# Performance work log

Measured on AMD Instinct MI355X. Metric: run time of the kernel, lower is better.

The kernel has to match this reference:

```python
import jax, jax.numpy as jnp
import numpy as np

B, D_IN, D_H = 262144, 128, 128
PROJ_EPS = 1e-5  # ball projection epsilon (c = 1.0)


def _norm(x):
    return jnp.linalg.norm(x, axis=-1, keepdims=True)


def logmap0(x):
    # atanh(||x||) * x / ||x||, safe at 0 (c = 1)
    n = _norm(x)
    ns = jnp.where(n == 0, 0.5, n)
    return jnp.where(n == 0, jnp.zeros_like(x), jnp.arctanh(ns) * x / ns)


def expmap0(v):
    # tanh(||v||) * v / ||v||, safe at 0 (c = 1)
    n = _norm(v)
    ns = jnp.where(n == 0, 1.0, n)
    return jnp.where(n == 0, jnp.zeros_like(v), jnp.tanh(ns) * v / ns)


def proj(x):
    # clip back inside the unit Poincare ball
    n = _norm(x)
    maxnorm = 1.0 - PROJ_EPS
    ns = jnp.where(n == 0, 1.0, n)
    return jnp.where(n > maxnorm, x / ns * maxnorm, x)


def setup_inputs() -> dict:
    key = jax.random.key(0)
    ks = jax.random.split(key, 8)
    scale = 0.03  # keep points well inside the ball: ||x|| ~ 0.03*sqrt(128) ~ 0.34
    x = scale * jax.random.normal(ks[0], (B, D_IN), dtype=jnp.float32)
    h = scale * jax.random.normal(ks[1], (B, D_H), dtype=jnp.float32)
    fan_in = D_IN + D_H
    w_std = 1.0 / np.sqrt(fan_in)
    Wr = w_std * jax.random.normal(ks[2], (fan_in, D_H), dtype=jnp.float32)
    br = w_std * jax.random.normal(ks[3], (D_H,), dtype=jnp.float32)
    Wz = w_std * jax.random.normal(ks[4], (fan_in, D_H), dtype=jnp.float32)
    bz = w_std * jax.random.normal(ks[5], (D_H,), dtype=jnp.float32)
    Wh = w_std * jax.random.normal(ks[6], (fan_in, D_H), dtype=jnp.float32)
    bh = w_std * jax.random.normal(ks[7], (D_H,), dtype=jnp.float32)
    return {"x": x, "h": h, "Wr": Wr, "br": br, "Wz": Wz, "bz": bz, "Wh": Wh, "bh": bh}


def reference(x, h, Wr, br, Wz, bz, Wh, bh):
    x_tan = logmap0(x)            # [B, D_IN]
    h_tan = logmap0(h)            # [B, D_H]
    xh = jnp.concatenate([x_tan, h_tan], axis=1)  # [B, D_IN+D_H]
    r = jax.nn.sigmoid(xh @ Wr + br)
    z = jax.nn.sigmoid(xh @ Wz + bz)
    xh_reset = jnp.concatenate([x_tan, r * h_tan], axis=1)
    h_tilde = jnp.tanh(xh_reset @ Wh + bh)
    h_new_tan = (1.0 - z) * h_tan + z * h_tilde
    return proj(expmap0(h_new_tan))  # [B, D_H]
```

## Files before the change

kernel.cpp:

```cpp
#include <hip/hip_runtime.h>
#include <hip/hip_bf16.h>

typedef __attribute__((ext_vector_type(4))) float f32x4;
typedef __attribute__((ext_vector_type(8))) short bf16x8;
typedef __attribute__((ext_vector_type(4))) short bf16x4;
typedef __attribute__((ext_vector_type(2))) unsigned int u32x2;

#define D 128
#define BM 64

__device__ __forceinline__ unsigned short f2bf(float f){
  union { float f; unsigned int i; } c; c.f = f;
  unsigned int i = c.i;
  i += 0x7fffu + ((i >> 16) & 1u);
  return (unsigned short)(i >> 16);
}
__device__ __forceinline__ float bf2f(unsigned short u){
  union { float f; unsigned int i; } c; c.i = ((unsigned int)u) << 16; return c.f;
}
__device__ __forceinline__ unsigned int pk2(float a, float b){
  __hip_bfloat162 t = __float22bfloat162_rn(make_float2(a, b));
  return *reinterpret_cast<unsigned int*>(&t);
}
__device__ __forceinline__ float rcp_f(float x){ return __builtin_amdgcn_rcpf(x); }
__device__ __forceinline__ float exp2_f(float x){ return __builtin_amdgcn_exp2f(x); }
__device__ __forceinline__ float sigmoid_f(float t){
  return rcp_f(1.0f + exp2_f(-1.442695041f * t));
}
__device__ __forceinline__ float tanh_f(float t){
  return __builtin_fmaf(2.0f, rcp_f(1.0f + exp2_f(-2.885390082f * t)), -1.0f);
}

__global__ void prep_weights(const float* __restrict__ Wr, const float* __restrict__ Wz,
                             const float* __restrict__ Wh, unsigned short* __restrict__ wp)
{
  int w = blockIdx.x >> 6;
  int f = blockIdx.x & 63;
  int l = threadIdx.x;
  const float* src = (w == 0) ? Wr : ((w == 1) ? Wz : Wh);
  int nf = f >> 3, kk = f & 7;
  int col = nf * 16 + (l & 15);
  int k0  = kk * 32 + (l >> 4) * 8;
  unsigned short* dst = wp + w * 32768 + (f * 64 + l) * 8;
#pragma unroll
  for (int j = 0; j < 8; ++j)
    dst[j] = f2bf(src[(k0 + j) * D + col]);
}

__global__ __launch_bounds__(256, 4) void gru_fused(
    const float* __restrict__ x, const float* __restrict__ h,
    const float* __restrict__ brp, const float* __restrict__ bzp, const float* __restrict__ bhp,
    const unsigned short* __restrict__ wp, float* __restrict__ out)
{
  __shared__ __align__(16) unsigned char A1[BM * 512];
  float* P = (float*)A1;

  const int tid = threadIdx.x;
  const int w   = tid >> 6;
  const int l   = tid & 63;
  const int l15 = l & 15;
  const int lq  = l >> 4;
  const size_t row0 = (size_t)blockIdx.x * BM;

  {
    const int row = tid >> 2;
    const int q   = tid & 3;
    const f32x4* xr = (const f32x4*)(x + (row0 + row) * D);
    const f32x4* hr = (const f32x4*)(h + (row0 + row) * D);
    f32x4 v[8];
    float ss = 0.f;
#pragma unroll
    for (int j = 0; j < 8; ++j){
      v[j] = xr[j * 4 + q];
      ss += v[j][0]*v[j][0] + v[j][1]*v[j][1] + v[j][2]*v[j][2] + v[j][3]*v[j][3];
    }
    ss += __shfl_xor(ss, 1, 64);
    ss += __shfl_xor(ss, 2, 64);
    float n = __builtin_amdgcn_sqrtf(ss);
    float s = 1.f;
    if (n > 1e-20f)
      s = 0.34657359f * __builtin_amdgcn_logf((1.f + n) * rcp_f(1.f - n)) * rcp_f(n);
#pragma unroll
    for (int j = 0; j < 8; ++j){
      unsigned int byte = (unsigned)(row * 512 + (4 * j + q) * 8) ^ (unsigned)((row & 7) << 4);
      u32x2 pk; pk[0] = pk2(v[j][0] * s, v[j][1] * s); pk[1] = pk2(v[j][2] * s, v[j][3] * s);
      *(u32x2*)(A1 + byte) = pk;
    }
    ss = 0.f;
#pragma unroll
    for (int j = 0; j < 8; ++j){
      v[j] = hr[j * 4 + q];
      ss += v[j][0]*v[j][0] + v[j][1]*v[j][1] + v[j][2]*v[j][2] + v[j][3]*v[j][3];
    }
    ss += __shfl_xor(ss, 1, 64);
    ss += __shfl_xor(ss, 2, 64);
    n = __builtin_amdgcn_sqrtf(ss);
    s = 1.f;
    if (n > 1e-20f)
      s = 0.34657359f * __builtin_amdgcn_logf((1.f + n) * rcp_f(1.f - n)) * rcp_f(n);
#pragma unroll
    for (int j = 0; j < 8; ++j){
      unsigned int byte = (unsigned)(row * 512 + 256 + (4 * j + q) * 8) ^ (unsigned)((row & 7) << 4);
      u32x2 pk; pk[0] = pk2(v[j][0] * s, v[j][1] * s); pk[1] = pk2(v[j][2] * s, v[j][3] * s);
      *(u32x2*)(A1 + byte) = pk;
    }
  }
  __syncthreads();

  const unsigned short* pwr = wp + w * 8192;
  const unsigned short* pwz = wp + 32768 + w * 8192;

  f32x4 ar0[4], ar1[4], az0[4], az1[4];
#pragma unroll
  for (int m = 0; m < 4; ++m){ ar0[m] = 0; ar1[m] = 0; az0[m] = 0; az1[m] = 0; }

#pragma unroll 2
  for (int kk = 0; kk < 8; ++kk){
    const bf16x8 wr0 = *(const bf16x8*)(pwr + kk * 512 + l * 8);
    const bf16x8 wr1 = *(const bf16x8*)(pwr + 4096 + kk * 512 + l * 8);
    const bf16x8 wz0 = *(const bf16x8*)(pwz + kk * 512 + l * 8);
    const bf16x8 wz1 = *(const bf16x8*)(pwz + 4096 + kk * 512 + l * 8);
#pragma unroll
    for (int m = 0; m < 4; ++m){
      const int row = m * 16 + l15;
      unsigned int byte = (unsigned)(row * 512 + (kk * 32 + lq * 8) * 2) ^ (unsigned)((row & 7) << 4);
      const bf16x8 b = *(const bf16x8*)(A1 + byte);
      ar0[m] = __builtin_amdgcn_mfma_f32_16x16x32_bf16(wr0, b, ar0[m], 0, 0, 0);
      ar1[m] = __builtin_amdgcn_mfma_f32_16x16x32_bf16(wr1, b, ar1[m], 0, 0, 0);
      az0[m] = __builtin_amdgcn_mfma_f32_16x16x32_bf16(wz0, b, az0[m], 0, 0, 0);
      az1[m] = __builtin_amdgcn_mfma_f32_16x16x32_bf16(wz1, b, az1[m], 0, 0, 0);
    }
  }

  const int c00 = w * 32 + lq * 4;
  const int c01 = c00 + 16;
  const f32x4 brv0 = *(const f32x4*)(brp + c00);
  const f32x4 brv1 = *(const f32x4*)(brp + c01);
  const f32x4 bzv0 = *(const f32x4*)(bzp + c00);
  const f32x4 bzv1 = *(const f32x4*)(bzp + c01);

  f32x4 zk0[4], zk1[4];
  u32x2 htp0[4], htp1[4];
  u32x2 rhp0[4], rhp1[4];
#pragma unroll
  for (int m = 0; m < 4; ++m){
    const int row = m * 16 + l15;
    const unsigned int swz = (unsigned)((row & 7) << 4);
    const bf16x4 h40 = *(const bf16x4*)(A1 + ((unsigned)(row * 512 + (128 + c00) * 2) ^ swz));
    const bf16x4 h41 = *(const bf16x4*)(A1 + ((unsigned)(row * 512 + (128 + c01) * 2) ^ swz));
    htp0[m] = *(const u32x2*)&h40;
    htp1[m] = *(const u32x2*)&h41;
    float rh0[4], rh1[4];
#pragma unroll
    for (int reg = 0; reg < 4; ++reg){
      float r0 = sigmoid_f(ar0[m][reg] + brv0[reg]);
      float r1 = sigmoid_f(ar1[m][reg] + brv1[reg]);
      zk0[m][reg] = sigmoid_f(az0[m][reg] + bzv0[reg]);
      zk1[m][reg] = sigmoid_f(az1[m][reg] + bzv1[reg]);
      rh0[reg] = r0 * bf2f((unsigned short)h40[reg]);
      rh1[reg] = r1 * bf2f((unsigned short)h41[reg]);
    }
    rhp0[m][0] = pk2(rh0[0], rh0[1]); rhp0[m][1] = pk2(rh0[2], rh0[3]);
    rhp1[m][0] = pk2(rh1[0], rh1[1]); rhp1[m][1] = pk2(rh1[2], rh1[3]);
  }
  __syncthreads();

#pragma unroll
  for (int m = 0; m < 4; ++m){
    const int row = m * 16 + l15;
    const unsigned int swz = (unsigned)((row & 7) << 4);
    *(u32x2*)(A1 + ((unsigned)(row * 512 + (128 + c00) * 2) ^ swz)) = rhp0[m];
    *(u32x2*)(A1 + ((unsigned)(row * 512 + (128 + c01) * 2) ^ swz)) = rhp1[m];
  }
  __syncthreads();

  const unsigned short* pwh = wp + 65536 + w * 8192;
  f32x4 ah0[4], ah1[4];
#pragma unroll
  for (int m = 0; m < 4; ++m){ ah0[m] = 0; ah1[m] = 0; }

#pragma unroll 2
  for (int kk = 0; kk < 8; ++kk){
    const bf16x8 wh0 = *(const bf16x8*)(pwh + kk * 512 + l * 8);
    const bf16x8 wh1 = *(const bf16x8*)(pwh + 4096 + kk * 512 + l * 8);
#pragma unroll
    for (int m = 0; m < 4; ++m){
      const int row = m * 16 + l15;
      unsigned int byte = (unsigned)(row * 512 + (kk * 32 + lq * 8) * 2) ^ (unsigned)((row & 7) << 4);
      const bf16x8 b = *(const bf16x8*)(A1 + byte);
      ah0[m] = __builtin_amdgcn_mfma_f32_16x16x32_bf16(wh0, b, ah0[m], 0, 0, 0);
      ah1[m] = __builtin_amdgcn_mfma_f32_16x16x32_bf16(wh1, b, ah1[m], 0, 0, 0);
    }
  }

  const f32x4 bhv0 = *(const f32x4*)(bhp + c00);
  const f32x4 bhv1 = *(const f32x4*)(bhp + c01);
  f32x4 o0[4], o1[4];
#pragma unroll
  for (int m = 0; m < 4; ++m){
#pragma unroll
    for (int reg = 0; reg < 4; ++reg){
      float htld0 = tanh_f(ah0[m][reg] + bhv0[reg]);
      float htld1 = tanh_f(ah1[m][reg] + bhv1[reg]);
      float ht0 = bf2f((unsigned short)(htp0[m][reg >> 1] >> ((reg & 1) * 16)));
      float ht1 = bf2f((unsigned short)(htp1[m][reg >> 1] >> ((reg & 1) * 16)));
      float z0 = zk0[m][reg], z1 = zk1[m][reg];
      o0[m][reg] = (1.f - z0) * ht0 + z0 * htld0;
      o1[m][reg] = (1.f - z1) * ht1 + z1 * htld1;
    }
  }
  __syncthreads();

#pragma unroll
  for (int m = 0; m < 4; ++m){
    const int row = m * 16 + l15;
    float s = 0.f;
#pragma unroll
    for (int reg = 0; reg < 4; ++reg)
      s += o0[m][reg]*o0[m][reg] + o1[m][reg]*o1[m][reg];
    s += __shfl_xor(s, 16, 64);
    s += __shfl_xor(s, 32, 64);
    if (lq == 0) P[row * 4 + w] = s;
  }
  __syncthreads();

#pragma unroll
  for (int m = 0; m < 4; ++m){
    const int row = m * 16 + l15;
    const f32x4 p4 = *(const f32x4*)(P + row * 4);
    float ss = p4[0] + p4[1] + p4[2] + p4[3];
    float n = __builtin_amdgcn_sqrtf(ss);
    float sc = 1.f;
    if (n > 1e-20f){
      float th = tanh_f(n);
      th = fminf(th, 0.99999f);
      sc = th * rcp_f(n);
    }
    float* orow = out + (row0 + row) * D;
    f32x4 st0 = o0[m] * sc;
    f32x4 st1 = o1[m] * sc;
    *(f32x4*)(orow + c00) = st0;
    *(f32x4*)(orow + c01) = st1;
  }
}

extern "C" void kernel_launch(void* const* d_in, const int* in_sizes, int n_in,
                              void* d_out, int out_size, void* d_ws, size_t ws_size,
                              hipStream_t stream)
{
  const float* x   = (const float*)d_in[0];
  const float* h   = (const float*)d_in[1];
  const float* Wr  = (const float*)d_in[2];
  const float* brp = (const float*)d_in[3];
  const float* Wz  = (const float*)d_in[4];
  const float* bzp = (const float*)d_in[5];
  const float* Wh  = (const float*)d_in[6];
  const float* bhp = (const float*)d_in[7];
  unsigned short* wsp = (unsigned short*)d_ws;

  prep_weights<<<192, 64, 0, stream>>>(Wr, Wz, Wh, wsp);
  gru_fused<<<262144 / BM, 256, 0, stream>>>(x, h, brp, bzp, bhp, wsp, (float*)d_out);
}
```

Measured before the change: 126.9 us.

## Prefetch weight fragments and split candidate GEMM to overlap the x-part with gating

```diff
diff --git a/kernel.cpp b/kernel.cpp
--- a/kernel.cpp
+++ b/kernel.cpp
@@ -62,6 +62,10 @@
   const int lq  = l >> 4;
   const size_t row0 = (size_t)blockIdx.x * BM;
 
+  const unsigned short* pwr = wp + w * 8192;
+  const unsigned short* pwz = wp + 32768 + w * 8192;
+  const unsigned short* pwh = wp + 65536 + w * 8192;
+
   {
     const int row = tid >> 2;
     const int q   = tid & 3;
@@ -105,21 +109,27 @@
       *(u32x2*)(A1 + byte) = pk;
     }
   }
-  __syncthreads();
-
-  const unsigned short* pwr = wp + w * 8192;
-  const unsigned short* pwz = wp + 32768 + w * 8192;
+
+  bf16x8 nwr0 = *(const bf16x8*)(pwr + 0 * 512 + l * 8);
+  bf16x8 nwr1 = *(const bf16x8*)(pwr + 4096 + 0 * 512 + l * 8);
+  bf16x8 nwz0 = *(const bf16x8*)(pwz + 0 * 512 + l * 8);
+  bf16x8 nwz1 = *(const bf16x8*)(pwz + 4096 + 0 * 512 + l * 8);
+
+  __syncthreads();
 
   f32x4 ar0[4], ar1[4], az0[4], az1[4];
 #pragma unroll
   for (int m = 0; m < 4; ++m){ ar0[m] = 0; ar1[m] = 0; az0[m] = 0; az1[m] = 0; }
 
-#pragma unroll 2
+#pragma unroll
   for (int kk = 0; kk < 8; ++kk){
-    const bf16x8 wr0 = *(const bf16x8*)(pwr + kk * 512 + l * 8);
-    const bf16x8 wr1 = *(const bf16x8*)(pwr + 4096 + kk * 512 + l * 8);
-    const bf16x8 wz0 = *(const bf16x8*)(pwz + kk * 512 + l * 8);
-    const bf16x8 wz1 = *(const bf16x8*)(pwz + 4096 + kk * 512 + l * 8);
+    const bf16x8 wr0 = nwr0, wr1 = nwr1, wz0 = nwz0, wz1 = nwz1;
+    if (kk < 7){
+      nwr0 = *(const bf16x8*)(pwr + (kk + 1) * 512 + l * 8);
+      nwr1 = *(const bf16x8*)(pwr + 4096 + (kk + 1) * 512 + l * 8);
+      nwz0 = *(const bf16x8*)(pwz + (kk + 1) * 512 + l * 8);
+      nwz1 = *(const bf16x8*)(pwz + 4096 + (kk + 1) * 512 + l * 8);
+    }
 #pragma unroll
     for (int m = 0; m < 4; ++m){
       const int row = m * 16 + l15;
@@ -163,6 +173,30 @@
     rhp0[m][0] = pk2(rh0[0], rh0[1]); rhp0[m][1] = pk2(rh0[2], rh0[3]);
     rhp1[m][0] = pk2(rh1[0], rh1[1]); rhp1[m][1] = pk2(rh1[2], rh1[3]);
   }
+
+  f32x4 ah0[4], ah1[4];
+#pragma unroll
+  for (int m = 0; m < 4; ++m){ ah0[m] = 0; ah1[m] = 0; }
+  bf16x8 nwh0 = *(const bf16x8*)(pwh + 0 * 512 + l * 8);
+  bf16x8 nwh1 = *(const bf16x8*)(pwh + 4096 + 0 * 512 + l * 8);
+#pragma unroll
+  for (int kk = 0; kk < 4; ++kk){
+    const bf16x8 wh0 = nwh0, wh1 = nwh1;
+    {
+      const int kn = (kk < 3) ? (kk + 1) : 4;
+      nwh0 = *(const bf16x8*)(pwh + kn * 512 + l * 8);
+      nwh1 = *(const bf16x8*)(pwh + 4096 + kn * 512 + l * 8);
+    }
+#pragma unroll
+    for (int m = 0; m < 4; ++m){
+      const int row = m * 16 + l15;
+      unsigned int byte = (unsigned)(row * 512 + (kk * 32 + lq * 8) * 2) ^ (unsigned)((row & 7) << 4);
+      const bf16x8 b = *(const bf16x8*)(A1 + byte);
+      ah0[m] = __builtin_amdgcn_mfma_f32_16x16x32_bf16(wh0, b, ah0[m], 0, 0, 0);
+      ah1[m] = __builtin_amdgcn_mfma_f32_16x16x32_bf16(wh1, b, ah1[m], 0, 0, 0);
+    }
+  }
+
   __syncthreads();
 
 #pragma unroll
@@ -174,15 +208,13 @@
   }
   __syncthreads();
 
-  const unsigned short* pwh = wp + 65536 + w * 8192;
-  f32x4 ah0[4], ah1[4];
-#pragma unroll
-  for (int m = 0; m < 4; ++m){ ah0[m] = 0; ah1[m] = 0; }
-
-#pragma unroll 2
-  for (int kk = 0; kk < 8; ++kk){
-    const bf16x8 wh0 = *(const bf16x8*)(pwh + kk * 512 + l * 8);
-    const bf16x8 wh1 = *(const bf16x8*)(pwh + 4096 + kk * 512 + l * 8);
+#pragma unroll
+  for (int kk = 4; kk < 8; ++kk){
+    const bf16x8 wh0 = nwh0, wh1 = nwh1;
+    if (kk < 7){
+      nwh0 = *(const bf16x8*)(pwh + (kk + 1) * 512 + l * 8);
+      nwh1 = *(const bf16x8*)(pwh + 4096 + (kk + 1) * 512 + l * 8);
+    }
 #pragma unroll
     for (int m = 0; m < 4; ++m){
       const int row = m * 16 + l15;
```

Result: slower. 219.5 us (+73.0%).
